# Optimization experiments

Hardware: AMD Instinct MI355X
Metric: run time of the kernel (lower is better)

## Reference

```python
import jax, jax.numpy as jnp
import numpy as np

B, T, N, FIN, D, LAG = 8, 64, 128, 64, 64, 8


def setup_inputs() -> dict:
    key = jax.random.key(0)
    ks = jax.random.split(key, 9)
    s_in = 0.05
    X = jax.random.normal(ks[0], (B, T, N, FIN), jnp.float32)
    Wq = jax.random.normal(ks[1], (FIN, D), jnp.float32) * s_in
    bq = jnp.zeros((D,), jnp.float32)
    Wk = jax.random.normal(ks[2], (FIN, D), jnp.float32) * s_in
    bk = jnp.zeros((D,), jnp.float32)
    Wv = jax.random.normal(ks[3], (FIN, D), jnp.float32) * s_in
    bv = jnp.zeros((D,), jnp.float32)
    Wo = jax.random.normal(ks[4], (2 * D, D), jnp.float32) * s_in
    bo = jnp.zeros((D,), jnp.float32)
    return {"X": X, "Wq": Wq, "bq": bq, "Wk": Wk, "bk": bk,
            "Wv": Wv, "bv": bv, "Wo": Wo, "bo": bo}


def reference(X, Wq, bq, Wk, bk, Wv, bv, Wo, bo):
    relu = jax.nn.relu
    Q = relu(jnp.einsum('btnf,fd->btnd', X, Wq) + bq)  # [B,T,N,D]
    K = relu(jnp.einsum('btnf,fd->btnd', X, Wk) + bk)
    V = relu(jnp.einsum('btnf,fd->btnd', X, Wv) + bv)

    pad = LAG - 1
    # Zero-pad time axis at the front so negative lags gather zeros
    # (faithful to the torch code: padded slots score 0 and still get
    #  softmax mass exp(0), they are NOT masked with -inf).
    Kp = jnp.pad(K, ((0, 0), (pad, 0), (0, 0), (0, 0)))
    Vp = jnp.pad(V, ((0, 0), (pad, 0), (0, 0), (0, 0)))
    # t_idx[t, l] = (t - l) + pad  -> index into padded time axis
    t_idx = jnp.arange(T)[:, None] - jnp.arange(LAG)[None, :] + pad  # [T,LAG]
    Kl = Kp[:, t_idx]  # [B,T,LAG,N,D]
    Vl = Vp[:, t_idx]  # [B,T,LAG,N,D]

    scale = 1.0 / jnp.sqrt(jnp.float32(D))
    scores = jnp.einsum('btnd,btlmd->btnlm', Q, Kl) * scale  # [B,T,N,LAG,N]
    scores = scores.reshape(B, T, N, LAG * N)
    w = jax.nn.softmax(scores, axis=-1)  # softmax over full lag-window KV
    agg = jnp.einsum('btnk,btkd->btnd', w, Vl.reshape(B, T, LAG * N, D))

    h = jnp.concatenate([Q, agg], axis=-1)  # [B,T,N,2D]
    out = relu(jnp.einsum('btnc,cd->btnd', h, Wo) + bo)
    # dropout is identity in eval mode
    return out
```

## Files before the change

### kernel.cpp

```cpp
#include <hip/hip_runtime.h>
#include <stdint.h>


typedef __bf16 bf16x8 __attribute__((ext_vector_type(8)));
typedef float f32x4 __attribute__((ext_vector_type(4)));

#define MFMA16(a, b, c) __builtin_amdgcn_mfma_f32_16x16x32_bf16((a), (b), (c), 0, 0, 0)

__device__ __forceinline__ unsigned short f2bf(float f) {
    union { float f; unsigned u; } v; v.f = f;
    unsigned r = v.u + 0x7FFFu + ((v.u >> 16) & 1u);
    return (unsigned short)(r >> 16);
}
__device__ __forceinline__ unsigned cvtpk(float lo, float hi) {
    unsigned r;
    asm("v_cvt_pk_bf16_f32 %0, %1, %2" : "=v"(r) : "v"(lo), "v"(hi));
    return r;
}
__device__ __forceinline__ float bflo(unsigned u) {
    union { unsigned x; float f; } v; v.x = u << 16; return v.f;
}
__device__ __forceinline__ float bfhi(unsigned u) {
    union { unsigned x; float f; } v; v.x = u & 0xffff0000u; return v.f;
}
__device__ __forceinline__ f32x4 fzero4() {
    f32x4 z; z[0] = 0.f; z[1] = 0.f; z[2] = 0.f; z[3] = 0.f; return z;
}

__global__ __launch_bounds__(256) void prep_kernel(
    const float* __restrict__ Wq, const float* __restrict__ Wk,
    const float* __restrict__ Wv, const float* __restrict__ Wo,
    unsigned short* __restrict__ WqT, unsigned short* __restrict__ WkT,
    unsigned short* __restrict__ WvT, unsigned short* __restrict__ WoT)
{
    __shared__ float lds[128][65];
    const int b = blockIdx.x, tid = threadIdx.x;
    const float* src = (b == 0) ? Wq : (b == 1) ? Wk : (b == 2) ? Wv : Wo;
    unsigned short* dst = (b == 0) ? WqT : (b == 1) ? WkT : (b == 2) ? WvT : WoT;
    const int n = (b == 3) ? 8192 : 4096;
    for (int i = tid; i < n; i += 256) lds[i >> 6][i & 63] = src[i];
    __syncthreads();
    if (b == 3) {
        for (int i = tid; i < 8192; i += 256) { int d = i >> 7, r = i & 127; dst[i] = f2bf(lds[r][d]); }
    } else {
        for (int i = tid; i < 4096; i += 256) { int d = i >> 6, r = i & 63;  dst[i] = f2bf(lds[r][d]); }
    }
}

__global__ __launch_bounds__(512, 2) void fused_kernel(
    const float* __restrict__ X,
    const unsigned short* __restrict__ WqT, const unsigned short* __restrict__ WkT,
    const unsigned short* __restrict__ WoT,
    const float* __restrict__ bq, const float* __restrict__ bk,
    const float* __restrict__ bv, const float* __restrict__ bo,
    float* __restrict__ Out)
{
    __shared__ __align__(16) unsigned char ldsKV[32768];
    __shared__ __align__(16) unsigned char ldsW[16384];

    const int tid = threadIdx.x;
    const int lane = tid & 63, wvid = tid >> 6;
    const int cl = lane & 15, g = lane >> 4;
    const int bt = ((blockIdx.x & 7) << 6) + (blockIdx.x >> 3);
    const int t = bt & 63;
    const int wq0 = wvid * 16;
    const int q = wq0 + cl;
    const int lo = (t < 7) ? 0 : (t - 7);
    const int swz = (cl & 7) << 4;

    unsigned char* bufK = ldsKV;
    unsigned char* bufV = ldsKV + 16384;

    {
        const uint4* w4 = (const uint4*)WkT;
#pragma unroll
        for (int j = 0; j < 2; ++j) {
            const int i = tid + j * 512;
            const int r = i >> 3, c0 = (i & 7) * 8;
            *(uint4*)(ldsW + ((r * 128 + c0 * 2) ^ ((r & 7) << 4))) = w4[i];
        }
    }

    uint2 bkp[4]; float bvs[4];
#pragma unroll
    for (int dt = 0; dt < 4; ++dt) {
        float4 b4 = *(const float4*)(bk + dt * 16 + g * 4);
        bkp[dt].x = cvtpk(b4.x, b4.y);
        bkp[dt].y = cvtpk(b4.z, b4.w);
        bvs[dt] = bv[dt * 16 + cl];
    }

    auto xchg = [&](unsigned a, unsigned b, unsigned& wl, unsigned& wh) {
        const int sl = cl + ((g & 1) << 5);
        unsigned ta = (unsigned)__shfl((int)a, sl, 64);
        unsigned tb = (unsigned)__shfl((int)b, sl, 64);
        unsigned ua = (unsigned)__shfl((int)a, sl + 16, 64);
        unsigned ub = (unsigned)__shfl((int)b, sl + 16, 64);
        wl = (g < 2) ? ta : tb;
        wh = (g < 2) ? ua : ub;
    };

    float4 xr0, xr1, xr2, xr3;
    {
        const float* xp = X + ((size_t)bt * 128 + q) * 64;
        xr0 = *(const float4*)(xp + g * 8);
        xr1 = *(const float4*)(xp + g * 8 + 4);
        xr2 = *(const float4*)(xp + 32 + g * 8);
        xr3 = *(const float4*)(xp + 32 + g * 8 + 4);
    }

    f32x4 o[4];
#pragma unroll
    for (int ni = 0; ni < 4; ++ni) o[ni] = fzero4();
    float lsum = 0.f;
    bf16x8 qf[2];

    for (int st = t; st >= lo; --st) {
        __syncthreads();

        bf16x8 xf[2];
        {
            unsigned u0 = cvtpk(xr0.x, xr0.y), u1 = cvtpk(xr0.z, xr0.w);
            unsigned u2 = cvtpk(xr1.x, xr1.y), u3 = cvtpk(xr1.z, xr1.w);
            unsigned wa[4] = {u0, u1, u2, u3};
            xf[0] = *(bf16x8*)wa;
            u0 = cvtpk(xr2.x, xr2.y); u1 = cvtpk(xr2.z, xr2.w);
            u2 = cvtpk(xr3.x, xr3.y); u3 = cvtpk(xr3.z, xr3.w);
            unsigned wb[4] = {u0, u1, u2, u3};
            xf[1] = *(bf16x8*)wb;
        }
        if (st > lo) {
            const float* xp = X + (((size_t)(bt - (t - st) - 1)) * 128 + q) * 64;
            xr0 = *(const float4*)(xp + g * 8);
            xr1 = *(const float4*)(xp + g * 8 + 4);
            xr2 = *(const float4*)(xp + 32 + g * 8);
            xr3 = *(const float4*)(xp + 32 + g * 8 + 4);
        }

#pragma unroll
        for (int dt = 0; dt < 4; ++dt) {
            const int rowK = dt * 16 + cl;
            const int rowV = 64 + dt * 16 + cl;
            bf16x8 wka = *(const bf16x8*)(ldsW + ((rowK * 128 + g * 16) ^ swz));
            bf16x8 wkb = *(const bf16x8*)(ldsW + ((rowK * 128 + 64 + g * 16) ^ swz));
            bf16x8 wva = *(const bf16x8*)(ldsW + ((rowV * 128 + g * 16) ^ swz));
            bf16x8 wvb = *(const bf16x8*)(ldsW + ((rowV * 128 + 64 + g * 16) ^ swz));
            f32x4 kacc = fzero4(), vacc = fzero4();
            kacc = MFMA16(wka, xf[0], kacc);
            kacc = MFMA16(wkb, xf[1], kacc);
            vacc = MFMA16(xf[0], wva, vacc);
            vacc = MFMA16(xf[1], wvb, vacc);
            {
                float k0 = fmaxf(kacc[0] + bflo(bkp[dt].x), 0.f);
                float k1 = fmaxf(kacc[1] + bfhi(bkp[dt].x), 0.f);
                float k2 = fmaxf(kacc[2] + bflo(bkp[dt].y), 0.f);
                float k3 = fmaxf(kacc[3] + bfhi(bkp[dt].y), 0.f);
                uint2 kp; kp.x = cvtpk(k0, k1); kp.y = cvtpk(k2, k3);
                *(uint2*)(bufK + ((q * 128 + (dt * 16 + g * 4) * 2) ^ swz)) = kp;
            }
            {
                const int d = dt * 16 + cl;
                float v0 = fmaxf(vacc[0] + bvs[dt], 0.f);
                float v1 = fmaxf(vacc[1] + bvs[dt], 0.f);
                float v2 = fmaxf(vacc[2] + bvs[dt], 0.f);
                float v3 = fmaxf(vacc[3] + bvs[dt], 0.f);
                uint2 vp; vp.x = cvtpk(v0, v1); vp.y = cvtpk(v2, v3);
                *(uint2*)(bufV + ((d * 256 + (wq0 + g * 4) * 2) ^ swz)) = vp;
            }
        }

        if (st == t) {
            unsigned qu[8];
#pragma unroll
            for (int dt = 0; dt < 4; ++dt) {
                const int rw = (dt * 16 + cl) * 64;
                bf16x8 wqa = *(const bf16x8*)(WqT + rw + g * 8);
                bf16x8 wqb = *(const bf16x8*)(WqT + rw + 32 + g * 8);
                f32x4 qacc = fzero4();
                qacc = MFMA16(wqa, xf[0], qacc);
                qacc = MFMA16(wqb, xf[1], qacc);
                float4 bq4 = *(const float4*)(bq + dt * 16 + g * 4);
                float q0 = fmaxf(qacc[0] + bq4.x, 0.f);
                float q1 = fmaxf(qacc[1] + bq4.y, 0.f);
                float q2 = fmaxf(qacc[2] + bq4.z, 0.f);
                float q3 = fmaxf(qacc[3] + bq4.w, 0.f);
                qu[2 * dt] = cvtpk(q0, q1);
                qu[2 * dt + 1] = cvtpk(q2, q3);
            }
#pragma unroll
            for (int kk = 0; kk < 2; ++kk) {
                unsigned w0, w1, w2, w3;
                xchg(qu[4 * kk], qu[4 * kk + 2], w0, w2);
                xchg(qu[4 * kk + 1], qu[4 * kk + 3], w1, w3);
                unsigned ww[4] = {w0, w1, w2, w3};
                qf[kk] = *(bf16x8*)ww;
            }
        }

        __syncthreads();

#pragma unroll
        for (int j = 0; j < 4; ++j) {
            const int keyA = (2 * j) * 16 + cl, keyB = keyA + 16;
            bf16x8 kfa0 = *(const bf16x8*)(bufK + ((keyA * 128 + g * 16) ^ swz));
            bf16x8 kfa1 = *(const bf16x8*)(bufK + ((keyA * 128 + 64 + g * 16) ^ swz));
            bf16x8 kfb0 = *(const bf16x8*)(bufK + ((keyB * 128 + g * 16) ^ swz));
            bf16x8 kfb1 = *(const bf16x8*)(bufK + ((keyB * 128 + 64 + g * 16) ^ swz));
            f32x4 sA = fzero4(), sB = fzero4();
            sA = MFMA16(kfa0, qf[0], sA);
            sA = MFMA16(kfa1, qf[1], sA);
            sB = MFMA16(kfb0, qf[0], sB);
            sB = MFMA16(kfb1, qf[1], sB);
            float pA0 = __expf(sA[0] * 0.125f), pA1 = __expf(sA[1] * 0.125f);
            float pA2 = __expf(sA[2] * 0.125f), pA3 = __expf(sA[3] * 0.125f);
            float pB0 = __expf(sB[0] * 0.125f), pB1 = __expf(sB[1] * 0.125f);
            float pB2 = __expf(sB[2] * 0.125f), pB3 = __expf(sB[3] * 0.125f);
            lsum += ((pA0 + pA1) + (pA2 + pA3)) + ((pB0 + pB1) + (pB2 + pB3));
            unsigned a0 = cvtpk(pA0, pA1), a1 = cvtpk(pA2, pA3);
            unsigned b0 = cvtpk(pB0, pB1), b1 = cvtpk(pB2, pB3);
            unsigned w0, w1, w2, w3;
            xchg(a0, b0, w0, w2);
            xchg(a1, b1, w1, w3);
            unsigned ww[4] = {w0, w1, w2, w3};
            bf16x8 pa = *(bf16x8*)ww;
#pragma unroll
            for (int ni = 0; ni < 4; ++ni) {
                const int d = ni * 16 + cl;
                bf16x8 vf = *(const bf16x8*)(bufV + ((d * 256 + (j * 32 + g * 8) * 2) ^ swz));
                o[ni] = MFMA16(pa, vf, o[ni]);
            }
        }
    }

    float ls = lsum;
    ls += __shfl_xor(ls, 16, 64);
    ls += __shfl_xor(ls, 32, 64);
    if (t < 7) ls += 128.0f * (float)(7 - t);
    float inv[4];
#pragma unroll
    for (int r = 0; r < 4; ++r) inv[r] = 1.0f / __shfl(ls, g * 4 + r, 64);

    __syncthreads();

    unsigned char* ldsH = ldsKV;
    unsigned char* ldsWo = ldsKV + 16384;
#pragma unroll
    for (int ni = 0; ni < 4; ++ni)
#pragma unroll
        for (int r = 0; r < 4; ++r) {
            const int qq = wq0 + g * 4 + r;
            const int d = ni * 16 + cl;
            *(unsigned short*)(ldsH + ((qq * 128 + d * 2) ^ ((qq & 7) << 4))) =
                f2bf(o[ni][r] * inv[r]);
        }

    {
        const uint4* wo4 = (const uint4*)WoT;
#pragma unroll
        for (int j = 0; j < 2; ++j) {
            const int i = tid + j * 512;
            const int d = i >> 4, c0 = (i & 15) * 8;
            *(uint4*)(ldsWo + ((d * 256 + c0 * 2) ^ ((d & 7) << 4))) = wo4[i];
        }
    }
    __syncthreads();

    f32x4 h2[4];
#pragma unroll
    for (int ni = 0; ni < 4; ++ni) h2[ni] = fzero4();
#pragma unroll
    for (int kk = 0; kk < 4; ++kk) {
        bf16x8 ha;
        if (kk < 2) {
            ha = qf[kk];
        } else {
            ha = *(const bf16x8*)(ldsH + ((q * 128 + ((kk - 2) * 32 + g * 8) * 2) ^ swz));
        }
#pragma unroll
        for (int ni = 0; ni < 4; ++ni) {
            const int dd = ni * 16 + cl;
            bf16x8 wb = *(const bf16x8*)(ldsWo + ((dd * 256 + (kk * 32 + g * 8) * 2) ^ swz));
            h2[ni] = MFMA16(ha, wb, h2[ni]);
        }
    }
#pragma unroll
    for (int ni = 0; ni < 4; ++ni) {
        const float b = bo[ni * 16 + cl];
#pragma unroll
        for (int r = 0; r < 4; ++r) {
            float v = h2[ni][r] + b;
            v = v > 0.f ? v : 0.f;
            Out[((size_t)bt * 128 + wq0 + g * 4 + r) * 64 + ni * 16 + cl] = v;
        }
    }
}

extern "C" void kernel_launch(void* const* d_in, const int* in_sizes, int n_in,
                              void* d_out, int out_size, void* d_ws, size_t ws_size,
                              hipStream_t stream) {
    const float* X  = (const float*)d_in[0];
    const float* Wq = (const float*)d_in[1];
    const float* bq = (const float*)d_in[2];
    const float* Wk = (const float*)d_in[3];
    const float* bk = (const float*)d_in[4];
    const float* Wv = (const float*)d_in[5];
    const float* bv = (const float*)d_in[6];
    const float* Wo = (const float*)d_in[7];
    const float* bo = (const float*)d_in[8];
    float* Out = (float*)d_out;

    unsigned short* WqT = (unsigned short*)d_ws;
    unsigned short* WkT = WqT + 4096;
    unsigned short* WvT = WqT + 8192;
    unsigned short* WoT = WqT + 12288;

    hipLaunchKernelGGL(prep_kernel, dim3(4), dim3(256), 0, stream,
                       Wq, Wk, Wv, Wo, WqT, WkT, WvT, WoT);
    hipLaunchKernelGGL(fused_kernel, dim3(512), dim3(512), 0, stream,
                       X, WqT, WkT, WoT, bq, bk, bv, bo, Out);
}
```

Measured before the change: 137.5 us.

## Permute K/V LDS column layout to drop cross-lane shuffles; keep Wk in registers

Stores K and V into shared memory with a permuted column order, with a matching permutation of Wo rows in the prep kernel. This lets the Q and softmax-probability fragments be fed straight into the MFMA without the four-shuffle exchange per fragment. The Wk fragments are also preloaded into registers once, so only Wv stays in LDS, which halves the weight LDS footprint and removes Wk LDS reads from the inner loop. The cost is more VGPR pressure under the 512x2 launch bounds.

Result: faster. 131.6 us (-4.2%).

```diff
diff --git a/kernel.cpp b/kernel.cpp
--- a/kernel.cpp
+++ b/kernel.cpp
@@ -41,7 +41,13 @@
     for (int i = tid; i < n; i += 256) lds[i >> 6][i & 63] = src[i];
     __syncthreads();
     if (b == 3) {
-        for (int i = tid; i < 8192; i += 256) { int d = i >> 7, r = i & 127; dst[i] = f2bf(lds[r][d]); }
+        for (int i = tid; i < 8192; i += 256) {
+            int d = i >> 7, c = i & 127;
+            int cs = (c < 64)
+                ? ((c & 32) | (((c >> 2) & 3) << 3) | (((c >> 4) & 1) << 2) | (c & 3))
+                : c;
+            dst[d * 128 + cs] = f2bf(lds[c][d]);
+        }
     } else {
         for (int i = tid; i < 4096; i += 256) { int d = i >> 6, r = i & 63;  dst[i] = f2bf(lds[r][d]); }
     }
@@ -50,13 +56,13 @@
 __global__ __launch_bounds__(512, 2) void fused_kernel(
     const float* __restrict__ X,
     const unsigned short* __restrict__ WqT, const unsigned short* __restrict__ WkT,
-    const unsigned short* __restrict__ WoT,
+    const unsigned short* __restrict__ WvT, const unsigned short* __restrict__ WoT,
     const float* __restrict__ bq, const float* __restrict__ bk,
     const float* __restrict__ bv, const float* __restrict__ bo,
     float* __restrict__ Out)
 {
     __shared__ __align__(16) unsigned char ldsKV[32768];
-    __shared__ __align__(16) unsigned char ldsW[16384];
+    __shared__ __align__(16) unsigned char ldsW[8192];
 
     const int tid = threadIdx.x;
     const int lane = tid & 63, wvid = tid >> 6;
@@ -72,14 +78,17 @@
     unsigned char* bufV = ldsKV + 16384;
 
     {
-        const uint4* w4 = (const uint4*)WkT;
-#pragma unroll
-        for (int j = 0; j < 2; ++j) {
-            const int i = tid + j * 512;
-            const int r = i >> 3, c0 = (i & 7) * 8;
-            *(uint4*)(ldsW + ((r * 128 + c0 * 2) ^ ((r & 7) << 4))) = w4[i];
-        }
-    }
+        const uint4* wv4 = (const uint4*)WvT;
+        const int r = tid >> 3, c0 = (tid & 7) * 8;
+        *(uint4*)(ldsW + ((r * 128 + c0 * 2) ^ ((r & 7) << 4))) = wv4[tid];
+    }
+
+    bf16x8 wkF[4][2];
+#pragma unroll
+    for (int dt = 0; dt < 4; ++dt)
+#pragma unroll
+        for (int kk = 0; kk < 2; ++kk)
+            wkF[dt][kk] = *(const bf16x8*)(WkT + (dt * 16 + cl) * 64 + kk * 32 + g * 8);
 
     uint2 bkp[4]; float bvs[4];
 #pragma unroll
@@ -89,16 +98,6 @@
         bkp[dt].y = cvtpk(b4.z, b4.w);
         bvs[dt] = bv[dt * 16 + cl];
     }
-
-    auto xchg = [&](unsigned a, unsigned b, unsigned& wl, unsigned& wh) {
-        const int sl = cl + ((g & 1) << 5);
-        unsigned ta = (unsigned)__shfl((int)a, sl, 64);
-        unsigned tb = (unsigned)__shfl((int)b, sl, 64);
-        unsigned ua = (unsigned)__shfl((int)a, sl + 16, 64);
-        unsigned ub = (unsigned)__shfl((int)b, sl + 16, 64);
-        wl = (g < 2) ? ta : tb;
-        wh = (g < 2) ? ua : ub;
-    };
 
     float4 xr0, xr1, xr2, xr3;
     {
@@ -139,33 +138,32 @@
 
 #pragma unroll
         for (int dt = 0; dt < 4; ++dt) {
-            const int rowK = dt * 16 + cl;
-            const int rowV = 64 + dt * 16 + cl;
-            bf16x8 wka = *(const bf16x8*)(ldsW + ((rowK * 128 + g * 16) ^ swz));
-            bf16x8 wkb = *(const bf16x8*)(ldsW + ((rowK * 128 + 64 + g * 16) ^ swz));
+            const int rowV = dt * 16 + cl;
             bf16x8 wva = *(const bf16x8*)(ldsW + ((rowV * 128 + g * 16) ^ swz));
             bf16x8 wvb = *(const bf16x8*)(ldsW + ((rowV * 128 + 64 + g * 16) ^ swz));
             f32x4 kacc = fzero4(), vacc = fzero4();
-            kacc = MFMA16(wka, xf[0], kacc);
-            kacc = MFMA16(wkb, xf[1], kacc);
+            kacc = MFMA16(wkF[dt][0], xf[0], kacc);
+            kacc = MFMA16(wkF[dt][1], xf[1], kacc);
             vacc = MFMA16(xf[0], wva, vacc);
             vacc = MFMA16(xf[1], wvb, vacc);
             {
+                const int colK = 32 * (dt >> 1) + 8 * g + 4 * (dt & 1);
                 float k0 = fmaxf(kacc[0] + bflo(bkp[dt].x), 0.f);
                 float k1 = fmaxf(kacc[1] + bfhi(bkp[dt].x), 0.f);
                 float k2 = fmaxf(kacc[2] + bflo(bkp[dt].y), 0.f);
                 float k3 = fmaxf(kacc[3] + bfhi(bkp[dt].y), 0.f);
                 uint2 kp; kp.x = cvtpk(k0, k1); kp.y = cvtpk(k2, k3);
-                *(uint2*)(bufK + ((q * 128 + (dt * 16 + g * 4) * 2) ^ swz)) = kp;
+                *(uint2*)(bufK + ((q * 128 + colK * 2) ^ swz)) = kp;
             }
             {
                 const int d = dt * 16 + cl;
+                const int colV = 32 * (wvid >> 1) + 8 * g + 4 * (wvid & 1);
                 float v0 = fmaxf(vacc[0] + bvs[dt], 0.f);
                 float v1 = fmaxf(vacc[1] + bvs[dt], 0.f);
                 float v2 = fmaxf(vacc[2] + bvs[dt], 0.f);
                 float v3 = fmaxf(vacc[3] + bvs[dt], 0.f);
                 uint2 vp; vp.x = cvtpk(v0, v1); vp.y = cvtpk(v2, v3);
-                *(uint2*)(bufV + ((d * 256 + (wq0 + g * 4) * 2) ^ swz)) = vp;
+                *(uint2*)(bufV + ((d * 256 + colV * 2) ^ swz)) = vp;
             }
         }
 
@@ -189,10 +187,7 @@
             }
 #pragma unroll
             for (int kk = 0; kk < 2; ++kk) {
-                unsigned w0, w1, w2, w3;
-                xchg(qu[4 * kk], qu[4 * kk + 2], w0, w2);
-                xchg(qu[4 * kk + 1], qu[4 * kk + 3], w1, w3);
-                unsigned ww[4] = {w0, w1, w2, w3};
+                unsigned ww[4] = {qu[4 * kk], qu[4 * kk + 1], qu[4 * kk + 2], qu[4 * kk + 3]};
                 qf[kk] = *(bf16x8*)ww;
             }
         }
@@ -216,12 +211,9 @@
             float pB0 = __expf(sB[0] * 0.125f), pB1 = __expf(sB[1] * 0.125f);
             float pB2 = __expf(sB[2] * 0.125f), pB3 = __expf(sB[3] * 0.125f);
             lsum += ((pA0 + pA1) + (pA2 + pA3)) + ((pB0 + pB1) + (pB2 + pB3));
-            unsigned a0 = cvtpk(pA0, pA1), a1 = cvtpk(pA2, pA3);
-            unsigned b0 = cvtpk(pB0, pB1), b1 = cvtpk(pB2, pB3);
-            unsigned w0, w1, w2, w3;
-            xchg(a0, b0, w0, w2);
-            xchg(a1, b1, w1, w3);
-            unsigned ww[4] = {w0, w1, w2, w3};
+            unsigned ww[4];
+            ww[0] = cvtpk(pA0, pA1); ww[1] = cvtpk(pA2, pA3);
+            ww[2] = cvtpk(pB0, pB1); ww[3] = cvtpk(pB2, pB3);
             bf16x8 pa = *(bf16x8*)ww;
 #pragma unroll
             for (int ni = 0; ni < 4; ++ni) {
@@ -317,5 +309,5 @@
     hipLaunchKernelGGL(prep_kernel, dim3(4), dim3(256), 0, stream,
                        Wq, Wk, Wv, Wo, WqT, WkT, WvT, WoT);
     hipLaunchKernelGGL(fused_kernel, dim3(512), dim3(512), 0, stream,
-                       X, WqT, WkT, WoT, bq, bk, bv, bo, Out);
-}
+                       X, WqT, WkT, WvT, WoT, bq, bk, bv, bo, Out);
+}
```
